# Kernel tuning notes

Hardware: AMD Instinct MI355X
Metric: run time of the kernel (lower is better)

## Reference

```python
import jax, jax.numpy as jnp
import numpy as np

D_MODEL = 2048
N_HEADS = 16
HEAD_DIM = D_MODEL // N_HEADS


def setup_inputs() -> dict:
    key = jax.random.key(0)
    ks = jax.random.split(key, 9)
    s = 0.02
    B, S = 4, 2048
    return {
        "x": jax.random.normal(ks[0], (B, S, D_MODEL), dtype=jnp.float32),
        "Wq": jax.random.normal(ks[1], (D_MODEL, D_MODEL), dtype=jnp.float32) * s,
        "bq": jnp.zeros((D_MODEL,), dtype=jnp.float32),
        "Wk": jax.random.normal(ks[2], (D_MODEL, D_MODEL), dtype=jnp.float32) * s,
        "bk": jnp.zeros((D_MODEL,), dtype=jnp.float32),
        "Wv": jax.random.normal(ks[3], (D_MODEL, D_MODEL), dtype=jnp.float32) * s,
        "bv": jnp.zeros((D_MODEL,), dtype=jnp.float32),
        "Wo": jax.random.normal(ks[4], (D_MODEL, D_MODEL), dtype=jnp.float32) * s,
        "bo": jnp.zeros((D_MODEL,), dtype=jnp.float32),
    }


def reference(x, Wq, bq, Wk, bk, Wv, bv, Wo, bo):
    B, S, _ = x.shape
    scale = jnp.asarray(np.sqrt(HEAD_DIM), dtype=x.dtype)

    def split_heads(t):  # [B,S,D] -> [B,H,S,hd]
        return t.reshape(B, S, N_HEADS, HEAD_DIM).transpose(0, 2, 1, 3)

    q = split_heads(x @ Wq + bq)
    k = split_heads(x @ Wk + bk)
    v = split_heads(x @ Wv + bv)

    # scores: [B,H,S,S]
    attn = jnp.einsum('bhqd,bhkd->bhqk', q, k) / scale
    kv_len = S
    causal = jnp.triu(jnp.ones((S, kv_len), dtype=bool), k=kv_len - S + 1)
    attn = jnp.where(causal[None, None], -jnp.inf, attn)
    attn = jax.nn.softmax(attn, axis=-1)
    # dropout is identity (p=0 / eval mode)
    out = jnp.einsum('bhqk,bhkd->bhqd', attn, v)
    out = out.transpose(0, 2, 1, 3).reshape(B, S, D_MODEL)
    return out @ Wo + bo
```

## Files before the change

### kernel.cpp

```cpp
#include <hip/hip_runtime.h>
#include <hip/hip_bf16.h>

#define DEV __device__ __forceinline__

typedef __bf16 bf16_t;
typedef __bf16 bf16x8 __attribute__((ext_vector_type(8)));
typedef __bf16 bf16x4 __attribute__((ext_vector_type(4)));
typedef float f32x4 __attribute__((ext_vector_type(4)));
typedef float f32x16 __attribute__((ext_vector_type(16)));
typedef unsigned int u32;
typedef unsigned short u16;
typedef u32 u32x4 __attribute__((ext_vector_type(4)));

constexpr int D_MODEL = 2048;
constexpr int SEQ = 2048;
constexpr int BATCH = 4;
constexpr int N_HEADS = 16;
constexpr int HEAD_DIM = 128;
constexpr int TOK = BATCH * SEQ;

DEV void gload_lds16(const void* g, void* l) {
  __builtin_amdgcn_global_load_lds(
      (const __attribute__((address_space(1))) unsigned int*)g,
      (__attribute__((address_space(3))) unsigned int*)l, 16, 0, 0);
}

DEV float fast_exp2(float x) {
#if __has_builtin(__builtin_amdgcn_exp2f)
  return __builtin_amdgcn_exp2f(x);
#else
  return exp2f(x);
#endif
}

DEV u32 pack2(float lo, float hi) {
  u16 a = __builtin_bit_cast(u16, (bf16_t)lo);
  u16 b = __builtin_bit_cast(u16, (bf16_t)hi);
  return (u32)a | ((u32)b << 16);
}

#define MFMA16(a, b, c) __builtin_amdgcn_mfma_f32_16x16x32_bf16((a), (b), (c), 0, 0, 0)
#define MFMA32(a, b, c) __builtin_amdgcn_mfma_f32_32x32x16_bf16((a), (b), (c), 0, 0, 0)

__global__ void k_cvt(const float* __restrict__ in, bf16_t* __restrict__ out, int n4) {
  int i = blockIdx.x * blockDim.x + threadIdx.x;
  int stride = gridDim.x * blockDim.x;
  for (; i < n4; i += stride) {
    float4 v = ((const float4*)in)[i];
    bf16x4 o;
    o[0] = (bf16_t)v.x; o[1] = (bf16_t)v.y; o[2] = (bf16_t)v.z; o[3] = (bf16_t)v.w;
    ((bf16x4*)out)[i] = o;
  }
}

__global__ void k_transpose_w4(const float* __restrict__ Wq, const float* __restrict__ Wk,
                               const float* __restrict__ Wv, const float* __restrict__ Wo,
                               bf16_t* __restrict__ WqkvT, bf16_t* __restrict__ WoT) {
  __shared__ float t[32][33];
  const int z = blockIdx.z;
  const float* W = z == 0 ? Wq : z == 1 ? Wk : z == 2 ? Wv : Wo;
  bf16_t* Wt = z < 3 ? WqkvT + (size_t)z * D_MODEL * D_MODEL : WoT;
  int k0 = blockIdx.x * 32, n0 = blockIdx.y * 32;
  int tx = threadIdx.x, ty = threadIdx.y;
#pragma unroll
  for (int r = ty; r < 32; r += 8)
    t[r][tx] = W[(size_t)(k0 + r) * D_MODEL + n0 + tx];
  __syncthreads();
#pragma unroll
  for (int r = ty; r < 32; r += 8)
    Wt[(size_t)(n0 + r) * D_MODEL + k0 + tx] = (bf16_t)t[tx][r];
}

template <int MODE>
__global__ __launch_bounds__(512, 2) void k_gemm256(const bf16_t* __restrict__ A,
                                                    const bf16_t* __restrict__ Bt,
                                                    const float* __restrict__ b0p,
                                                    const float* __restrict__ b1p,
                                                    const float* __restrict__ b2p,
                                                    void* __restrict__ o0,
                                                    void* __restrict__ o1,
                                                    void* __restrict__ o2) {
  constexpr int K = D_MODEL;
  constexpr int NTOT = (MODE == 0) ? 3 * D_MODEL : D_MODEL;
  constexpr int NT = K / 64;
  __shared__ __attribute__((aligned(16))) bf16_t sh[2][2][2][8192];

  const int bid = blockIdx.x;
  const int nbn = NTOT / 256;
  const int cpx = gridDim.x >> 3;
  const int swz = (bid & 7) * cpx + (bid >> 3);
  const int bm = swz / nbn, bn = swz % nbn;

  const int tid = threadIdx.x;
  const int lane = tid & 63;
  const int w = tid >> 6;
  const int wm = w >> 2, wn = w & 3;
  const int lr = lane & 15, lg = lane >> 4;

  const bf16_t* Agl[2];
  const bf16_t* Bgl[2];
  int ldsg[2];
#pragma unroll
  for (int l = 0; l < 2; ++l) {
    int g = l * 512 + tid;
    int r = g >> 2, c = g & 3;
    int csw = c ^ ((r ^ (r >> 2)) & 3);
    Agl[l] = A + (size_t)(bm * 256 + r) * K + csw * 8;
    Bgl[l] = Bt + (size_t)(bn * 256 + r) * K + csw * 8;
    ldsg[l] = g * 8;
  }

  auto SA = [&](int buf, int t, int kh) {
    const int off = t * 64 + kh * 32;
#pragma unroll
    for (int l = 0; l < 2; ++l) gload_lds16(Agl[l] + off, &sh[buf][0][kh][ldsg[l]]);
  };
  auto SB = [&](int buf, int t, int kh) {
    const int off = t * 64 + kh * 32;
#pragma unroll
    for (int l = 0; l < 2; ++l) gload_lds16(Bgl[l] + off, &sh[buf][1][kh][ldsg[l]]);
  };

  int offA[8], offB[4];
  const int cx = lg ^ ((lr ^ (lr >> 2)) & 3);
#pragma unroll
  for (int i = 0; i < 8; ++i) offA[i] = (wm * 128 + i * 16 + lr) * 32 + cx * 8;
#pragma unroll
  for (int j = 0; j < 4; ++j) offB[j] = (wn * 64 + j * 16 + lr) * 32 + cx * 8;

  f32x4 acc[8][4] = {};
  bf16x8 af[8], bf_[4];

  SA(0, 0, 0); SB(0, 0, 0); SA(0, 0, 1); SB(0, 0, 1);

#define MFMA_ROW(i)                                  \
  acc[i][0] = MFMA16(af[i], bf_[0], acc[i][0]);      \
  acc[i][1] = MFMA16(af[i], bf_[1], acc[i][1]);      \
  acc[i][2] = MFMA16(af[i], bf_[2], acc[i][2]);      \
  acc[i][3] = MFMA16(af[i], bf_[3], acc[i][3]);

  for (int t = 0; t < NT; ++t) {
    const int cur = t & 1, nxt = cur ^ 1;
    const int t1 = (t + 1 < NT) ? t + 1 : NT - 1;
#pragma unroll
    for (int kh = 0; kh < 2; ++kh) {
      asm volatile("s_waitcnt vmcnt(4)" ::: "memory");
      __builtin_amdgcn_s_barrier();
#pragma unroll
      for (int j = 0; j < 4; ++j) bf_[j] = *(const bf16x8*)&sh[cur][1][kh][offB[j]];
#pragma unroll
      for (int i = 0; i < 8; ++i) af[i] = *(const bf16x8*)&sh[cur][0][kh][offA[i]];
      SA(nxt, t1, kh);
      SB(nxt, t1, kh);
      __builtin_amdgcn_s_setprio(1);
      asm volatile("s_waitcnt lgkmcnt(6)" ::: "memory");
      __builtin_amdgcn_sched_barrier(0);
      MFMA_ROW(0) MFMA_ROW(1)
      asm volatile("s_waitcnt lgkmcnt(4)" ::: "memory");
      __builtin_amdgcn_sched_barrier(0);
      MFMA_ROW(2) MFMA_ROW(3)
      asm volatile("s_waitcnt lgkmcnt(2)" ::: "memory");
      __builtin_amdgcn_sched_barrier(0);
      MFMA_ROW(4) MFMA_ROW(5)
      asm volatile("s_waitcnt lgkmcnt(0)" ::: "memory");
      __builtin_amdgcn_sched_barrier(0);
      MFMA_ROW(6) MFMA_ROW(7)
      __builtin_amdgcn_s_setprio(0);
    }
  }
#undef MFMA_ROW

  asm volatile("s_waitcnt vmcnt(0) lgkmcnt(0)" ::: "memory");

#pragma unroll
  for (int i = 0; i < 8; ++i) {
    const int row = bm * 256 + wm * 128 + i * 16 + lg * 4;
#pragma unroll
    for (int jn = 0; jn < 4; ++jn) {
      const int col = bn * 256 + wn * 64 + jn * 16 + lr;
      if (MODE == 1) {
        const float bv = b0p[col];
        float* Cf = (float*)o0;
#pragma unroll
        for (int j = 0; j < 4; ++j)
          Cf[(size_t)(row + j) * D_MODEL + col] = acc[i][jn][j] + bv;
      } else {
        const int sel = col >> 11, cl = col & 2047;
        const float bv = (sel == 0 ? b0p : sel == 1 ? b1p : b2p)[cl];
        if (sel < 2) {
          bf16_t* dst = (bf16_t*)(sel == 0 ? o0 : o1);
#pragma unroll
          for (int j = 0; j < 4; ++j)
            dst[(size_t)(row + j) * D_MODEL + cl] = (bf16_t)(acc[i][jn][j] + bv);
        } else {
          const int bb2 = row >> 11, s = row & 2047;
          bf16x4 ov;
#pragma unroll
          for (int j = 0; j < 4; ++j) ov[j] = (bf16_t)(acc[i][jn][j] + bv);
          bf16_t* Vt = (bf16_t*)o2;
          *(bf16x4*)(Vt + (((size_t)(bb2 * 16 + (cl >> 7))) * 128 + (cl & 127)) * 2048 + s) = ov;
        }
      }
    }
  }
}

__global__ __launch_bounds__(256, 3) void k_attn(const bf16_t* __restrict__ Q,
                                                 const bf16_t* __restrict__ K,
                                                 const bf16_t* __restrict__ Vt,
                                                 bf16_t* __restrict__ AO) {
  const int fid = blockIdx.x;
  const int qb = 15 - (fid >> 6);
  const int bh = fid & 63;
  const int b = bh >> 4, h = bh & 15;
  const int w = threadIdx.x >> 6, lane = threadIdx.x & 63;
  const int l31 = lane & 31, hl = lane >> 5;
  const int nt = 4 * qb + 4;

  __shared__ __attribute__((aligned(16))) bf16_t Ks[2][32 * 128];
  __shared__ __attribute__((aligned(16))) bf16_t Vs[2][128 * 32];

  const bf16_t* kbase = K + (size_t)(b * SEQ) * D_MODEL + h * HEAD_DIM;
  const bf16_t* vtbase = Vt + (size_t)bh * HEAD_DIM * SEQ;
  const float C = 0.12751949848078418f;

  auto STAGE = [&](int buf, int kt) {
    const int tt = threadIdx.x;
#pragma unroll
    for (int p = 0; p < 2; ++p) {
      int g = p * 256 + tt;
      int r = g >> 4, c = g & 15;
      gload_lds16(kbase + (size_t)(kt * 32 + r) * D_MODEL + ((c ^ (r & 7)) * 8),
                  &Ks[buf][(size_t)(g & ~63) * 8]);
    }
#pragma unroll
    for (int p = 0; p < 2; ++p) {
      int g = p * 256 + tt;
      int r = g >> 2, c = g & 3;
      gload_lds16(vtbase + (size_t)r * SEQ + kt * 32 + ((c ^ ((r ^ (r >> 2)) & 3)) * 8),
                  &Vs[buf][(size_t)(g & ~63) * 8]);
    }
  };

  const int qw0 = qb * 128 + w * 32;
  const int qa = qw0 + l31;

  const bf16_t* qp = Q + (size_t)(b * SEQ + qa) * D_MODEL + h * HEAD_DIM + hl * 8;
  bf16x8 qf[8];
#pragma unroll
  for (int step = 0; step < 8; ++step) qf[step] = *(const bf16x8*)(qp + step * 16);

  f32x16 oacc[4];
#pragma unroll
  for (int db = 0; db < 4; ++db)
#pragma unroll
    for (int r = 0; r < 16; ++r) oacc[db][r] = 0.f;
  float m = -1e30f, lsum = 0.f;

  STAGE(0, 0);
  asm volatile("s_waitcnt vmcnt(0)" ::: "memory");
  __syncthreads();

  int buf = 0;
  for (int kt = 0; kt < nt; ++kt) {
    if (kt + 1 < nt) STAGE(buf ^ 1, kt + 1);

    if (kt * 32 < qw0 + 32) {
      f32x16 sacc;
#pragma unroll
      for (int r = 0; r < 16; ++r) sacc[r] = 0.f;
      const bf16_t* kr = &Ks[buf][l31 * 128];
      const int rx = l31 & 7;
      __builtin_amdgcn_s_setprio(1);
#pragma unroll
      for (int step = 0; step < 8; ++step) {
        bf16x8 kf = *(const bf16x8*)(kr + (((step * 2 + hl) ^ rx) * 8));
        sacc = MFMA32(kf, qf[step], sacc);
      }
      __builtin_amdgcn_s_setprio(0);

      const bool domask = (kt * 32 + 31 > qw0);
#pragma unroll
      for (int r = 0; r < 16; ++r) {
        float v = sacc[r] * C;
        if (domask) {
          int kv = kt * 32 + 4 * hl + (r & 3) + 8 * (r >> 2);
          if (kv > qa) v = -1e30f;
        }
        sacc[r] = v;
      }
      float mx8[8];
#pragma unroll
      for (int r = 0; r < 8; ++r) mx8[r] = fmaxf(sacc[r], sacc[r + 8]);
#pragma unroll
      for (int r = 0; r < 4; ++r) mx8[r] = fmaxf(mx8[r], mx8[r + 4]);
      float tm = fmaxf(fmaxf(mx8[0], mx8[1]), fmaxf(mx8[2], mx8[3]));
      tm = fmaxf(tm, __shfl_xor(tm, 32));

      if (!__all(tm <= m + 11.5f)) {
        const float mn = fmaxf(m, tm);
        const float al = fast_exp2(m - mn);
        lsum *= al;
#pragma unroll
        for (int db = 0; db < 4; ++db)
#pragma unroll
          for (int r = 0; r < 16; ++r) oacc[db][r] *= al;
        m = mn;
      }

#pragma unroll
      for (int r = 0; r < 16; ++r) sacc[r] = fast_exp2(sacc[r] - m);
      float sm8[8];
#pragma unroll
      for (int r = 0; r < 8; ++r) sm8[r] = sacc[r] + sacc[r + 8];
#pragma unroll
      for (int r = 0; r < 4; ++r) sm8[r] = sm8[r] + sm8[r + 4];
      float ls = (sm8[0] + sm8[1]) + (sm8[2] + sm8[3]);
      lsum += ls + __shfl_xor(ls, 32);

      bf16x8 pb[2];
#pragma unroll
      for (int ck = 0; ck < 2; ++ck) {
        u32 a0 = pack2(sacc[8 * ck + 0], sacc[8 * ck + 1]);
        u32 a1 = pack2(sacc[8 * ck + 2], sacc[8 * ck + 3]);
        u32 b0 = pack2(sacc[8 * ck + 4], sacc[8 * ck + 5]);
        u32 b1 = pack2(sacc[8 * ck + 6], sacc[8 * ck + 7]);
        u32 send0 = hl ? a0 : b0, send1 = hl ? a1 : b1;
        u32 keep0 = hl ? b0 : a0, keep1 = hl ? b1 : a1;
        u32 r0 = __shfl_xor(send0, 32), r1 = __shfl_xor(send1, 32);
        u32x4 fv;
        fv[0] = hl ? r0 : keep0;
        fv[1] = hl ? r1 : keep1;
        fv[2] = hl ? keep0 : r0;
        fv[3] = hl ? keep1 : r1;
        pb[ck] = __builtin_bit_cast(bf16x8, fv);
      }

      __builtin_amdgcn_s_setprio(1);
#pragma unroll
      for (int db = 0; db < 4; ++db) {
        const int vrow = db * 32 + l31;
        const bf16_t* vr = &Vs[buf][vrow * 32];
        const int vx = (vrow ^ (vrow >> 2)) & 3;
#pragma unroll
        for (int ck = 0; ck < 2; ++ck) {
          bf16x8 vf = *(const bf16x8*)(vr + (((ck * 2 + hl) ^ vx) * 8));
          oacc[db] = MFMA32(vf, pb[ck], oacc[db]);
        }
      }
      __builtin_amdgcn_s_setprio(0);
    }

    __syncthreads();
    buf ^= 1;
  }

  const float inv = 1.f / lsum;
  bf16_t* ao = AO + (size_t)(b * SEQ + qa) * D_MODEL + h * HEAD_DIM;
#pragma unroll
  for (int db = 0; db < 4; ++db)
#pragma unroll
    for (int g = 0; g < 4; ++g) {
      bf16x4 ov;
#pragma unroll
      for (int j = 0; j < 4; ++j) ov[j] = (bf16_t)(oacc[db][4 * g + j] * inv);
      *(bf16x4*)(ao + db * 32 + 8 * g + 4 * hl) = ov;
    }
}

extern "C" void kernel_launch(void* const* d_in, const int* in_sizes, int n_in,
                              void* d_out, int out_size, void* d_ws, size_t ws_size,
                              hipStream_t stream) {
  const float* x  = (const float*)d_in[0];
  const float* Wq = (const float*)d_in[1];
  const float* bq = (const float*)d_in[2];
  const float* Wk = (const float*)d_in[3];
  const float* bk = (const float*)d_in[4];
  const float* Wv = (const float*)d_in[5];
  const float* bv = (const float*)d_in[6];
  const float* Wo = (const float*)d_in[7];
  const float* bo = (const float*)d_in[8];

  const size_t SZ_X = (size_t)TOK * D_MODEL * sizeof(bf16_t);
  const size_t SZ_W = (size_t)D_MODEL * D_MODEL * sizeof(bf16_t);

  char* p = (char*)d_ws;
  bf16_t* xb    = (bf16_t*)p;                     p += SZ_X;
  bf16_t* WqkvT = (bf16_t*)p;                     p += 3 * SZ_W;
  bf16_t* WoT   = (bf16_t*)p;                     p += SZ_W;
  bf16_t* Qm    = (bf16_t*)p;                     p += SZ_X;
  bf16_t* Km    = (bf16_t*)p;                     p += SZ_X;
  bf16_t* Vt    = (bf16_t*)p;                     p += SZ_X;
  bf16_t* AO    = xb;

  k_cvt<<<2048, 256, 0, stream>>>(x, xb, TOK * D_MODEL / 4);

  dim3 tb(32, 8);
  k_transpose_w4<<<dim3(64, 64, 4), tb, 0, stream>>>(Wq, Wk, Wv, Wo, WqkvT, WoT);

  const int gqkv = (TOK / 256) * (3 * D_MODEL / 256);
  k_gemm256<0><<<gqkv, 512, 0, stream>>>(xb, WqkvT, bq, bk, bv, Qm, Km, Vt);

  k_attn<<<1024, 256, 0, stream>>>(Qm, Km, Vt, AO);

  const int go = (TOK / 256) * (D_MODEL / 256);
  k_gemm256<1><<<go, 512, 0, stream>>>(AO, WoT, bo, nullptr, nullptr, d_out, nullptr, nullptr);
}
```

Before: 420.1 us.

## Restructure GEMM main loop into ping-pong quarter phases with extra barriers

Reworks the 256x256 GEMM K-loop so each k-half is split into two phases, each loading four A fragments and issuing one global-to-LDS load. The phases are fenced by s_barrier calls with setprio around the MFMA blocks, in the style of a ping-pong schedule where the two waves per SIMD alternate between memory and MFMA work. This reduces live fragment registers and is meant to interleave loads with compute across waves. In exchange it adds about four barriers per k-half, and lgkmcnt(0) waits before each MFMA block remove the finer-grained overlap of LDS reads with MFMAs.

```diff
diff --git a/kernel.cpp b/kernel.cpp
--- a/kernel.cpp
+++ b/kernel.cpp
@@ -83,7 +83,8 @@
   constexpr int K = D_MODEL;
   constexpr int NTOT = (MODE == 0) ? 3 * D_MODEL : D_MODEL;
   constexpr int NT = K / 64;
-  __shared__ __attribute__((aligned(16))) bf16_t sh[2][2][2][8192];
+  __shared__ __attribute__((aligned(16))) bf16_t shA[2][2][8192];
+  __shared__ __attribute__((aligned(16))) bf16_t shB[2][2][8192];
 
   const int bid = blockIdx.x;
   const int nbn = NTOT / 256;
@@ -110,15 +111,15 @@
     ldsg[l] = g * 8;
   }
 
-  auto SA = [&](int buf, int t, int kh) {
+  auto SAh = [&](int buf, int t, int kh) {
     const int off = t * 64 + kh * 32;
 #pragma unroll
-    for (int l = 0; l < 2; ++l) gload_lds16(Agl[l] + off, &sh[buf][0][kh][ldsg[l]]);
+    for (int l = 0; l < 2; ++l) gload_lds16(Agl[l] + off, &shA[buf][kh][ldsg[l]]);
   };
-  auto SB = [&](int buf, int t, int kh) {
+  auto SBh = [&](int buf, int t, int kh) {
     const int off = t * 64 + kh * 32;
 #pragma unroll
-    for (int l = 0; l < 2; ++l) gload_lds16(Bgl[l] + off, &sh[buf][1][kh][ldsg[l]]);
+    for (int l = 0; l < 2; ++l) gload_lds16(Bgl[l] + off, &shB[buf][kh][ldsg[l]]);
   };
 
   int offA[8], offB[4];
@@ -129,46 +130,76 @@
   for (int j = 0; j < 4; ++j) offB[j] = (wn * 64 + j * 16 + lr) * 32 + cx * 8;
 
   f32x4 acc[8][4] = {};
-  bf16x8 af[8], bf_[4];
-
-  SA(0, 0, 0); SB(0, 0, 0); SA(0, 0, 1); SB(0, 0, 1);
-
-#define MFMA_ROW(i)                                  \
-  acc[i][0] = MFMA16(af[i], bf_[0], acc[i][0]);      \
-  acc[i][1] = MFMA16(af[i], bf_[1], acc[i][1]);      \
-  acc[i][2] = MFMA16(af[i], bf_[2], acc[i][2]);      \
-  acc[i][3] = MFMA16(af[i], bf_[3], acc[i][3]);
+  bf16x8 aq[4], bq[4];
+
+  SAh(0, 0, 0); SBh(0, 0, 0); SAh(0, 0, 1); SBh(0, 0, 1);
+  asm volatile("s_waitcnt vmcnt(4)" ::: "memory");
+  __builtin_amdgcn_s_barrier();
+
+#define MFMA_Q(base)                                        \
+  _Pragma("unroll")                                         \
+  for (int i = 0; i < 4; ++i) {                             \
+    acc[base + i][0] = MFMA16(aq[i], bq[0], acc[base + i][0]); \
+    acc[base + i][1] = MFMA16(aq[i], bq[1], acc[base + i][1]); \
+    acc[base + i][2] = MFMA16(aq[i], bq[2], acc[base + i][2]); \
+    acc[base + i][3] = MFMA16(aq[i], bq[3], acc[base + i][3]); \
+  }
 
   for (int t = 0; t < NT; ++t) {
     const int cur = t & 1, nxt = cur ^ 1;
     const int t1 = (t + 1 < NT) ? t + 1 : NT - 1;
-#pragma unroll
-    for (int kh = 0; kh < 2; ++kh) {
-      asm volatile("s_waitcnt vmcnt(4)" ::: "memory");
-      __builtin_amdgcn_s_barrier();
-#pragma unroll
-      for (int j = 0; j < 4; ++j) bf_[j] = *(const bf16x8*)&sh[cur][1][kh][offB[j]];
-#pragma unroll
-      for (int i = 0; i < 8; ++i) af[i] = *(const bf16x8*)&sh[cur][0][kh][offA[i]];
-      SA(nxt, t1, kh);
-      SB(nxt, t1, kh);
-      __builtin_amdgcn_s_setprio(1);
-      asm volatile("s_waitcnt lgkmcnt(6)" ::: "memory");
-      __builtin_amdgcn_sched_barrier(0);
-      MFMA_ROW(0) MFMA_ROW(1)
-      asm volatile("s_waitcnt lgkmcnt(4)" ::: "memory");
-      __builtin_amdgcn_sched_barrier(0);
-      MFMA_ROW(2) MFMA_ROW(3)
-      asm volatile("s_waitcnt lgkmcnt(2)" ::: "memory");
-      __builtin_amdgcn_sched_barrier(0);
-      MFMA_ROW(4) MFMA_ROW(5)
-      asm volatile("s_waitcnt lgkmcnt(0)" ::: "memory");
-      __builtin_amdgcn_sched_barrier(0);
-      MFMA_ROW(6) MFMA_ROW(7)
-      __builtin_amdgcn_s_setprio(0);
-    }
-  }
-#undef MFMA_ROW
+
+#pragma unroll
+    for (int j = 0; j < 4; ++j) bq[j] = *(const bf16x8*)&shB[cur][0][offB[j]];
+#pragma unroll
+    for (int i = 0; i < 4; ++i) aq[i] = *(const bf16x8*)&shA[cur][0][offA[i]];
+    SAh(nxt, t1, 0);
+    __builtin_amdgcn_s_barrier();
+    asm volatile("s_waitcnt lgkmcnt(0)" ::: "memory");
+    __builtin_amdgcn_sched_barrier(0);
+    __builtin_amdgcn_s_setprio(1);
+    MFMA_Q(0)
+    __builtin_amdgcn_s_setprio(0);
+    __builtin_amdgcn_s_barrier();
+
+#pragma unroll
+    for (int i = 0; i < 4; ++i) aq[i] = *(const bf16x8*)&shA[cur][0][offA[i + 4]];
+    SBh(nxt, t1, 0);
+    __builtin_amdgcn_s_barrier();
+    asm volatile("s_waitcnt lgkmcnt(0)" ::: "memory");
+    __builtin_amdgcn_sched_barrier(0);
+    __builtin_amdgcn_s_setprio(1);
+    MFMA_Q(4)
+    __builtin_amdgcn_s_setprio(0);
+    asm volatile("s_waitcnt vmcnt(4)" ::: "memory");
+    __builtin_amdgcn_s_barrier();
+
+#pragma unroll
+    for (int j = 0; j < 4; ++j) bq[j] = *(const bf16x8*)&shB[cur][1][offB[j]];
+#pragma unroll
+    for (int i = 0; i < 4; ++i) aq[i] = *(const bf16x8*)&shA[cur][1][offA[i]];
+    SAh(nxt, t1, 1);
+    __builtin_amdgcn_s_barrier();
+    asm volatile("s_waitcnt lgkmcnt(0)" ::: "memory");
+    __builtin_amdgcn_sched_barrier(0);
+    __builtin_amdgcn_s_setprio(1);
+    MFMA_Q(0)
+    __builtin_amdgcn_s_setprio(0);
+    __builtin_amdgcn_s_barrier();
+
+#pragma unroll
+    for (int i = 0; i < 4; ++i) aq[i] = *(const bf16x8*)&shA[cur][1][offA[i + 4]];
+    SBh(nxt, t1, 1);
+    __builtin_amdgcn_s_barrier();
+    asm volatile("s_waitcnt lgkmcnt(0)" ::: "memory");
+    __builtin_amdgcn_sched_barrier(0);
+    __builtin_amdgcn_s_setprio(1);
+    MFMA_Q(4)
+    __builtin_amdgcn_s_setprio(0);
+    asm volatile("s_waitcnt vmcnt(4)" ::: "memory");
+    __builtin_amdgcn_s_barrier();
+  }
+#undef MFMA_Q
 
   asm volatile("s_waitcnt vmcnt(0) lgkmcnt(0)" ::: "memory");
 
```

Measured after the change: 459.1 us. 1.09x slower.
